# Kernel tuning notes

Hardware: AMD Instinct MI355X
Metric: run time of the kernel (lower is better)

The kernel has to match this reference:

```python
import jax, jax.numpy as jnp
import numpy as np

D_OUT, D_IN = 4096, 11008
REMAINED = 5504            # int(D_IN * 0.5)
N_CLUSTERS = 64


def setup_inputs() -> dict:
    key = jax.random.key(0)
    k1, k2, k3, k4 = jax.random.split(key, 4)
    x = jax.random.normal(k1, (1, REMAINED), dtype=jnp.float32)
    weight = jax.random.normal(k2, (D_OUT, D_IN), dtype=jnp.float32) * 0.02
    bias = jax.random.normal(k3, (D_OUT,), dtype=jnp.float32) * 0.02
    act_idx = jax.random.randint(k4, (N_CLUSTERS, REMAINED), 0, D_IN, dtype=jnp.int64)
    return {"x": x, "weight": weight, "bias": bias, "act_idx": act_idx, "cluster": 3}


def reference(x, weight, bias, act_idx, cluster):
    # Decode (batch=1) path of ReduceLayer_fc2:
    # gather the activated columns for this cluster, then GEMV + bias.
    cols = act_idx[cluster]                 # [R] indices into d_in
    filtered_w = weight[:, cols]            # [D_out, R] column gather
    return x @ filtered_w.T + bias          # [1, D_out]
```

## Files before the change

kernel.cpp:

```cpp
#include <hip/hip_runtime.h>

constexpr int D_OUT    = 4096;
constexpr int D_IN     = 11008;
constexpr int REMAINED = 5504;
constexpr int NV       = D_IN / 4;
constexpr int BLK      = 256;
constexpr int ROWS     = 8;

typedef float fvec4 __attribute__((ext_vector_type(4)));

__global__ __launch_bounds__(BLK) void fused_gemv_kernel(
    const float* __restrict__ x,
    const fvec4* __restrict__ W,
    const float* __restrict__ bias,
    const int*   __restrict__ act_idx,
    const int*   __restrict__ cluster,
    float*       __restrict__ out)
{
    __shared__ float xd[D_IN];
    __shared__ float red[ROWS][BLK / 64];

    const int tid  = threadIdx.x;
    const int row0 = blockIdx.x * ROWS;
    const fvec4* w0 = W + (size_t)row0 * NV;

    fvec4 wpre[ROWS];
    #pragma unroll
    for (int r = 0; r < ROWS; ++r)
        wpre[r] = __builtin_nontemporal_load(&w0[(size_t)r * NV + tid]);

    fvec4* xdw = (fvec4*)xd;
    for (int i = tid; i < NV; i += BLK) xdw[i] = (fvec4)0.f;
    __syncthreads();

    const int c = cluster[0];
    const int4*  idx4 = (const int4*) (act_idx + (size_t)c * REMAINED);
    const fvec4* x4   = (const fvec4*)x;
    for (int i = tid; i < REMAINED / 4; i += BLK) {
        int4  id = idx4[i];
        fvec4 xv = x4[i];
        atomicAdd(&xd[id.x], xv.x);
        atomicAdd(&xd[id.y], xv.y);
        atomicAdd(&xd[id.z], xv.z);
        atomicAdd(&xd[id.w], xv.w);
    }
    __syncthreads();

    const fvec4* xd4 = (const fvec4*)xd;
    float acc[ROWS] = {};
    {
        fvec4 xv = xd4[tid];
        #pragma unroll
        for (int r = 0; r < ROWS; ++r)
            acc[r] = fmaf(wpre[r].x, xv.x, fmaf(wpre[r].y, xv.y,
                     fmaf(wpre[r].z, xv.z, fmaf(wpre[r].w, xv.w, acc[r]))));
    }
    for (int k = tid + BLK; k < NV; k += BLK) {
        fvec4 xv = xd4[k];
        #pragma unroll
        for (int r = 0; r < ROWS; ++r) {
            fvec4 w = __builtin_nontemporal_load(&w0[(size_t)r * NV + k]);
            acc[r] = fmaf(w.x, xv.x, fmaf(w.y, xv.y,
                     fmaf(w.z, xv.z, fmaf(w.w, xv.w, acc[r]))));
        }
    }

    const int lane = tid & 63;
    const int wave = tid >> 6;
    #pragma unroll
    for (int r = 0; r < ROWS; ++r) {
        float v = acc[r];
        #pragma unroll
        for (int off = 32; off > 0; off >>= 1)
            v += __shfl_down(v, off, 64);
        if (lane == 0) red[r][wave] = v;
    }
    __syncthreads();
    if (tid < ROWS) {
        float s = red[tid][0] + red[tid][1] + red[tid][2] + red[tid][3];
        out[row0 + tid] = s + bias[row0 + tid];
    }
}

extern "C" void kernel_launch(void* const* d_in, const int* in_sizes, int n_in,
                              void* d_out, int out_size, void* d_ws, size_t ws_size,
                              hipStream_t stream)
{
    const float* x       = (const float*)d_in[0];
    const float* weight  = (const float*)d_in[1];
    const float* bias    = (const float*)d_in[2];
    const int*   act_idx = (const int*)d_in[3];
    const int*   cluster = (const int*)d_in[4];
    float*       out     = (float*)d_out;

    fused_gemv_kernel<<<D_OUT / ROWS, BLK, 0, stream>>>(
        x, (const fvec4*)weight, bias, act_idx, cluster, out);
}
```

Baseline: 251.4 us.

## Double-buffer weight loads in registers and prefetch scatter indices early

The kernel now loads the cluster's indices and x values into registers before the weight prefetch. The GEMV loop is restructured to hold two register buffers of weight vectors (wA/wB), refilling one while computing on the other, with a fixed trip count and an explicit tail. A launch_bounds occupancy hint of 2 blocks is added. The goal is to keep more HBM loads in flight and hide latency behind the shared-memory scatter, at the cost of higher register pressure.

Measured after the change: 245.4 us. 2.4% less time.

```diff
diff --git a/kernel.cpp b/kernel.cpp
--- a/kernel.cpp
+++ b/kernel.cpp
@@ -6,10 +6,12 @@
 constexpr int NV       = D_IN / 4;
 constexpr int BLK      = 256;
 constexpr int ROWS     = 8;
+constexpr int NIDX4    = REMAINED / 4;
+constexpr int ISLOT    = (NIDX4 + BLK - 1) / BLK;
 
 typedef float fvec4 __attribute__((ext_vector_type(4)));
 
-__global__ __launch_bounds__(BLK) void fused_gemv_kernel(
+__global__ __launch_bounds__(BLK, 2) void fused_gemv_kernel(
     const float* __restrict__ x,
     const fvec4* __restrict__ W,
     const float* __restrict__ bias,
@@ -24,46 +26,82 @@
     const int row0 = blockIdx.x * ROWS;
     const fvec4* w0 = W + (size_t)row0 * NV;
 
-    fvec4 wpre[ROWS];
+    const int c = cluster[0];
+    const int4*  idx4 = (const int4*)(act_idx + (size_t)c * REMAINED);
+    const fvec4* x4   = (const fvec4*)x;
+    int4  idreg[ISLOT];
+    fvec4 xreg[ISLOT];
+    #pragma unroll
+    for (int s = 0; s < ISLOT; ++s) {
+        const int i = tid + s * BLK;
+        if (i < NIDX4) { xreg[s] = x4[i]; idreg[s] = idx4[i]; }
+    }
+
+    fvec4 wA[ROWS], wB[ROWS];
     #pragma unroll
     for (int r = 0; r < ROWS; ++r)
-        wpre[r] = __builtin_nontemporal_load(&w0[(size_t)r * NV + tid]);
+        wA[r] = __builtin_nontemporal_load(&w0[(size_t)r * NV + tid]);
+    #pragma unroll
+    for (int r = 0; r < ROWS; ++r)
+        wB[r] = __builtin_nontemporal_load(&w0[(size_t)r * NV + tid + BLK]);
 
     fvec4* xdw = (fvec4*)xd;
     for (int i = tid; i < NV; i += BLK) xdw[i] = (fvec4)0.f;
     __syncthreads();
 
-    const int c = cluster[0];
-    const int4*  idx4 = (const int4*) (act_idx + (size_t)c * REMAINED);
-    const fvec4* x4   = (const fvec4*)x;
-    for (int i = tid; i < REMAINED / 4; i += BLK) {
-        int4  id = idx4[i];
-        fvec4 xv = x4[i];
-        atomicAdd(&xd[id.x], xv.x);
-        atomicAdd(&xd[id.y], xv.y);
-        atomicAdd(&xd[id.z], xv.z);
-        atomicAdd(&xd[id.w], xv.w);
+    #pragma unroll
+    for (int s = 0; s < ISLOT; ++s) {
+        const int i = tid + s * BLK;
+        if (i < NIDX4) {
+            atomicAdd(&xd[idreg[s].x], xreg[s].x);
+            atomicAdd(&xd[idreg[s].y], xreg[s].y);
+            atomicAdd(&xd[idreg[s].z], xreg[s].z);
+            atomicAdd(&xd[idreg[s].w], xreg[s].w);
+        }
     }
     __syncthreads();
 
     const fvec4* xd4 = (const fvec4*)xd;
     float acc[ROWS] = {};
-    {
-        fvec4 xv = xd4[tid];
+
+    #define FMA8(wv, xv) do { _Pragma("unroll")                                 \
+        for (int r = 0; r < ROWS; ++r)                                          \
+            acc[r] = fmaf((wv)[r].x, (xv).x, fmaf((wv)[r].y, (xv).y,            \
+                     fmaf((wv)[r].z, (xv).z, fmaf((wv)[r].w, (xv).w, acc[r])))); \
+        } while (0)
+
+    int kc = tid;
+    #pragma unroll 1
+    for (int it = 0; it < 4; ++it) {
+        fvec4 xv0 = xd4[kc];
+        FMA8(wA, xv0);
         #pragma unroll
         for (int r = 0; r < ROWS; ++r)
-            acc[r] = fmaf(wpre[r].x, xv.x, fmaf(wpre[r].y, xv.y,
-                     fmaf(wpre[r].z, xv.z, fmaf(wpre[r].w, xv.w, acc[r]))));
+            wA[r] = __builtin_nontemporal_load(&w0[(size_t)r * NV + kc + 2 * BLK]);
+        fvec4 xv1 = xd4[kc + BLK];
+        FMA8(wB, xv1);
+        #pragma unroll
+        for (int r = 0; r < ROWS; ++r)
+            wB[r] = __builtin_nontemporal_load(&w0[(size_t)r * NV + kc + 3 * BLK]);
+        kc += 2 * BLK;
     }
-    for (int k = tid + BLK; k < NV; k += BLK) {
-        fvec4 xv = xd4[k];
-        #pragma unroll
-        for (int r = 0; r < ROWS; ++r) {
-            fvec4 w = __builtin_nontemporal_load(&w0[(size_t)r * NV + k]);
-            acc[r] = fmaf(w.x, xv.x, fmaf(w.y, xv.y,
-                     fmaf(w.z, xv.z, fmaf(w.w, xv.w, acc[r]))));
+    {
+        fvec4 xv0 = xd4[kc];
+        FMA8(wA, xv0);
+        const bool tail = (tid < NV - 10 * BLK);
+        if (tail) {
+            #pragma unroll
+            for (int r = 0; r < ROWS; ++r)
+                wA[r] = __builtin_nontemporal_load(&w0[(size_t)r * NV + kc + 2 * BLK]);
+        }
+        fvec4 xv1 = xd4[kc + BLK];
+        FMA8(wB, xv1);
+        if (tail) {
+            fvec4 xv2 = xd4[kc + 2 * BLK];
+            FMA8(wA, xv2);
         }
     }
+    #undef FMA8
 
     const int lane = tid & 63;
     const int wave = tid >> 6;
```
